# Optimization experiments

Measured on AMD Instinct MI355X. Metric: run time of the kernel, lower is better.

The kernel has to match this reference:

```python
import jax, jax.numpy as jnp
import numpy as np

B, S, D, H = 4, 2048, 1024, 4096  # batch, seq, d_model, mlp hidden
EPS = 1e-12  # F.normalize eps


def _linear(x, W, b):
    return x @ W.T + b


def setup_inputs() -> dict:
    key = jax.random.key(0)
    ks = jax.random.split(key, 14)
    s = lambda d: 1.0 / np.sqrt(d)
    return {
        "x": jax.random.normal(ks[0], (B, S, D), dtype=jnp.float32),
        "Wq": jax.random.normal(ks[1], (D, D), dtype=jnp.float32) * s(D),
        "bq": jax.random.normal(ks[2], (D,), dtype=jnp.float32) * 0.01,
        "Wk": jax.random.normal(ks[3], (D, D), dtype=jnp.float32) * s(D),
        "bk": jax.random.normal(ks[4], (D,), dtype=jnp.float32) * 0.01,
        "Wv": jax.random.normal(ks[5], (D, D), dtype=jnp.float32) * s(D),
        "bv": jax.random.normal(ks[6], (D,), dtype=jnp.float32) * 0.01,
        "W1": jax.random.normal(ks[7], (D, D), dtype=jnp.float32) * s(D),
        "b1": jax.random.normal(ks[8], (D,), dtype=jnp.float32) * 0.01,
        "W2": jax.random.normal(ks[9], (H, D), dtype=jnp.float32) * s(D),
        "b2": jax.random.normal(ks[10], (H,), dtype=jnp.float32) * 0.01,
        "W3": jax.random.normal(ks[11], (D, H), dtype=jnp.float32) * s(H),
        "b3": jax.random.normal(ks[12], (D,), dtype=jnp.float32) * 0.01,
    }


def reference(x, Wq, bq, Wk, bk, Wv, bv, W1, b1, W2, b2, W3, b3):
    Q = _linear(x, Wq, bq)  # [B,S,D]
    K = _linear(x, Wk, bk)
    V = _linear(x, Wv, bv)
    # L2-normalize along feature dim (F.normalize, p=2, dim=2)
    Q = Q / jnp.maximum(jnp.linalg.norm(Q, axis=2, keepdims=True), EPS)
    K = K / jnp.maximum(jnp.linalg.norm(K, axis=2, keepdims=True), EPS)
    sim = jnp.einsum("bqd,bkd->bqk", Q, K)  # cosine similarities [B,S,S]
    attn = jax.nn.softmax(sim, axis=2)
    out = jnp.einsum("bqk,bkd->bqd", attn, V)  # [B,S,D]
    # MLP: Linear->relu->Linear->relu->Linear (dropout identity in eval)
    h = jax.nn.relu(_linear(out, W1, b1))
    h = jax.nn.relu(_linear(h, W2, b2))
    return _linear(h, W3, b3)
```

## Files before the change

### kernel.cpp

```cpp
#include <hip/hip_runtime.h>


using u16 = unsigned short;
using bf16x8 = __attribute__((ext_vector_type(8))) __bf16;
using f32x4  = __attribute__((ext_vector_type(4))) float;

__device__ __forceinline__ u16 f2bf(float f) {
  unsigned u = __float_as_uint(f);
  unsigned r = (u + 0x7FFFu + ((u >> 16) & 1u)) >> 16;
  return (u16)r;
}
__device__ __forceinline__ float bf2f(u16 h) {
  return __uint_as_float(((unsigned)h) << 16);
}

__device__ __forceinline__ void decomp(int lid, int nwg, int gx, int gy,
                                       int gby, int& bx, int& by, int& bz) {
  const int q = nwg >> 3, r = nwg & 7;
  const int xcd = lid & 7, jj = lid >> 3;
  const int wg = (xcd < r ? xcd * (q + 1) : r * (q + 1) + (xcd - r) * q) + jj;
  const int byloc = wg % gby;
  const int t1 = wg / gby;
  bx = t1 % gx;
  const int t2 = t1 / gx;
  const int nb = gy / gby;
  const int band = t2 % nb;
  bz = t2 / nb;
  by = band * gby + byloc;
}

struct CastSegs {
  const float* src[7];
  u16* dst[7];
  long beg[8];
};
__global__ __launch_bounds__(256) void cast_multi_kernel(CastSegs cs) {
  long idx = (long)blockIdx.x * 256 + threadIdx.x;
  if (idx >= cs.beg[7]) return;
  int seg = 0;
#pragma unroll
  for (int s = 1; s < 7; ++s) seg += (idx >= cs.beg[s]) ? 1 : 0;
  const long loc = idx - cs.beg[seg];
  float4 v = reinterpret_cast<const float4*>(cs.src[seg])[loc];
  ushort4 o;
  o.x = f2bf(v.x); o.y = f2bf(v.y); o.z = f2bf(v.z); o.w = f2bf(v.w);
  reinterpret_cast<ushort4*>(cs.dst[seg])[loc] = o;
}

__global__ __launch_bounds__(256) void l2norm2_kernel(
    const u16* __restrict__ Qi, const u16* __restrict__ Ki,
    u16* __restrict__ Qo, u16* __restrict__ Ko) {
  __shared__ float red[4];
  long row = blockIdx.x;
  const u16* in;
  u16* out;
  if (row < 8192) { in = Qi + row * 1024; out = Qo + row * 1024; }
  else            { in = Ki + (row - 8192) * 1024; out = Ko + (row - 8192) * 1024; }
  const int tid = threadIdx.x, lane = tid & 63, wave = tid >> 6;
  ushort4 h = *reinterpret_cast<const ushort4*>(in + tid * 4);
  float x0 = bf2f(h.x), x1 = bf2f(h.y), x2 = bf2f(h.z), x3 = bf2f(h.w);
  float ss = x0 * x0 + x1 * x1 + x2 * x2 + x3 * x3;
#pragma unroll
  for (int o = 32; o; o >>= 1) ss += __shfl_xor(ss, o);
  if (lane == 0) red[wave] = ss;
  __syncthreads();
  ss = red[0] + red[1] + red[2] + red[3];
  float s = 1.0f / fmaxf(sqrtf(ss), 1e-12f);
  ushort4 o;
  o.x = f2bf(x0 * s); o.y = f2bf(x1 * s); o.z = f2bf(x2 * s); o.w = f2bf(x3 * s);
  *reinterpret_cast<ushort4*>(out + tid * 4) = o;
}

__global__ void transpose_kernel(const u16* __restrict__ in, u16* __restrict__ out,
                                 int rows, int cols) {
  __shared__ u16 t[32][33];
  const int c0 = blockIdx.x * 32, r0 = blockIdx.y * 32;
  const long off = (long)blockIdx.z * rows * cols;
  const u16* ib = in + off;
  u16* ob = out + off;
  const int tx = threadIdx.x, ty = threadIdx.y;
#pragma unroll
  for (int j = 0; j < 4; ++j)
    t[ty + j * 8][tx] = ib[(long)(r0 + ty + j * 8) * cols + c0 + tx];
  __syncthreads();
#pragma unroll
  for (int j = 0; j < 4; ++j)
    ob[(long)(c0 + ty + j * 8) * rows + r0 + tx] = t[tx][ty + j * 8];
}

__global__ __launch_bounds__(256) void softmax_kernel(
    const u16* __restrict__ in, u16* __restrict__ out) {
  __shared__ float red[4];
  long row = blockIdx.x;
  const int tid = threadIdx.x, lane = tid & 63, wave = tid >> 6;
  const u16* p = in + row * 2048 + tid * 8;
  ushort4 h0 = *reinterpret_cast<const ushort4*>(p);
  ushort4 h1 = *reinterpret_cast<const ushort4*>(p + 4);
  float v[8];
  v[0] = bf2f(h0.x); v[1] = bf2f(h0.y); v[2] = bf2f(h0.z); v[3] = bf2f(h0.w);
  v[4] = bf2f(h1.x); v[5] = bf2f(h1.y); v[6] = bf2f(h1.z); v[7] = bf2f(h1.w);
  float m = v[0];
#pragma unroll
  for (int i = 1; i < 8; ++i) m = fmaxf(m, v[i]);
#pragma unroll
  for (int o = 32; o; o >>= 1) m = fmaxf(m, __shfl_xor(m, o));
  if (lane == 0) red[wave] = m;
  __syncthreads();
  m = fmaxf(fmaxf(red[0], red[1]), fmaxf(red[2], red[3]));
  float s = 0.0f;
#pragma unroll
  for (int i = 0; i < 8; ++i) { v[i] = __expf(v[i] - m); s += v[i]; }
#pragma unroll
  for (int o = 32; o; o >>= 1) s += __shfl_xor(s, o);
  __syncthreads();
  if (lane == 0) red[wave] = s;
  __syncthreads();
  s = red[0] + red[1] + red[2] + red[3];
  float inv = 1.0f / s;
  ushort4 o0, o1;
  o0.x = f2bf(v[0] * inv); o0.y = f2bf(v[1] * inv);
  o0.z = f2bf(v[2] * inv); o0.w = f2bf(v[3] * inv);
  o1.x = f2bf(v[4] * inv); o1.y = f2bf(v[5] * inv);
  o1.z = f2bf(v[6] * inv); o1.w = f2bf(v[7] * inv);
  *reinterpret_cast<ushort4*>(out + row * 2048 + tid * 8) = o0;
  *reinterpret_cast<ushort4*>(out + row * 2048 + tid * 8 + 4) = o1;
}

struct Frags { bf16x8 a[4][2]; bf16x8 b[4][2]; };

template <int MODE>
__global__ __launch_bounds__(256, 2) void gemmo(
    const u16* __restrict__ A, const u16* __restrict__ Bw,
    const float* __restrict__ bias, void* __restrict__ Cout,
    const float* __restrict__ bias2, void* __restrict__ Cout2,
    const float* __restrict__ bias3, void* __restrict__ Cout3,
    int N, int K, long batchA, long batchB, long batchC, int relu,
    int gx, int gy, int gby) {
  constexpr int ASZ = 128 * 64;
  constexpr int BSZ = 128 * 64;
  __shared__ u16 lds[2 * (ASZ + BSZ)];
  u16* const ldsA = lds;
  u16* const ldsB = lds + 2 * ASZ;

  int bx, by, bz;
  decomp(blockIdx.x, gridDim.x, gx, gy, gby, bx, by, bz);

  const int tid = threadIdx.x, wave = tid >> 6, lane = tid & 63;
  const int wr = wave >> 1, wc = wave & 1;
  const int fr = lane & 15, hi = lane >> 4;

  const long Abase = bz * batchA + (long)by * 128 * K;
  const long Bbase = bz * batchB + (long)bx * 128 * K;

  int aoff[4][2], boff[4][2];
#pragma unroll
  for (int m = 0; m < 4; ++m) {
    const int row = wr * 64 + m * 16 + fr;
#pragma unroll
    for (int ks = 0; ks < 2; ++ks)
      aoff[m][ks] = row * 64 + (((ks * 4 + hi) ^ (row & 7)) * 8);
  }
#pragma unroll
  for (int n = 0; n < 4; ++n) {
    const int row = wc * 64 + n * 16 + fr;
#pragma unroll
    for (int ks = 0; ks < 2; ++ks)
      boff[n][ks] = row * 64 + (((ks * 4 + hi) ^ (row & 7)) * 8);
  }

  const int rA = tid >> 3;
  const int g8 = (((tid & 7) ^ ((tid >> 3) & 7)) * 8);
  long asrc[4], bsrc[4];
#pragma unroll
  for (int rr = 0; rr < 4; ++rr) {
    asrc[rr] = Abase + (long)(rr * 32 + rA) * K + g8;
    bsrc[rr] = Bbase + (long)(rr * 32 + rA) * K + g8;
  }

#define STAGE_A(bufp, rr, k0)                                                  \
  __builtin_amdgcn_global_load_lds(                                            \
      (const __attribute__((address_space(1))) void*)(A + asrc[rr] + (k0)),    \
      (__attribute__((address_space(3))) void*)((bufp) + (rr) * 2048 + tid * 8), \
      16, 0, 0)
#define STAGE_B(bufp, rr, k0)                                                  \
  __builtin_amdgcn_global_load_lds(                                            \
      (const __attribute__((address_space(1))) void*)(Bw + bsrc[rr] + (k0)),   \
      (__attribute__((address_space(3))) void*)((bufp) + (rr) * 2048 + tid * 8), \
      16, 0, 0)
#define STAGE_TILE(T)                                                          \
  {                                                                            \
    u16* sA_ = ldsA + ((T) & 1) * ASZ;                                         \
    u16* sB_ = ldsB + ((T) & 1) * BSZ;                                         \
    const int k0_ = (T) << 6;                                                  \
    STAGE_A(sA_, 0, k0_); STAGE_A(sA_, 1, k0_);                                \
    STAGE_A(sA_, 2, k0_); STAGE_A(sA_, 3, k0_);                                \
    STAGE_B(sB_, 0, k0_); STAGE_B(sB_, 1, k0_);                                \
    STAGE_B(sB_, 2, k0_); STAGE_B(sB_, 3, k0_);                                \
  }
#define READ_FRAGS(F, T)                                                       \
  {                                                                            \
    u16* rA_ = ldsA + ((T) & 1) * ASZ;                                         \
    u16* rB_ = ldsB + ((T) & 1) * BSZ;                                         \
    _Pragma("unroll") for (int m = 0; m < 4; ++m)                              \
    _Pragma("unroll") for (int ks = 0; ks < 2; ++ks)                           \
      F.a[m][ks] = *reinterpret_cast<const bf16x8*>(&rA_[aoff[m][ks]]);        \
    _Pragma("unroll") for (int n = 0; n < 4; ++n)                              \
    _Pragma("unroll") for (int ks = 0; ks < 2; ++ks)                           \
      F.b[n][ks] = *reinterpret_cast<const bf16x8*>(&rB_[boff[n][ks]]);        \
  }
#define RA_ITER(T, FC, FN)                                                     \
  {                                                                            \
    if ((T) + 2 < NT) STAGE_TILE((T) + 2)                                      \
    if ((T) + 1 < NT) {                                                        \
      if ((T) + 2 < NT) asm volatile("s_waitcnt vmcnt(8)" ::: "memory");       \
      else              asm volatile("s_waitcnt vmcnt(0)" ::: "memory");       \
      __builtin_amdgcn_s_barrier();                                            \
      READ_FRAGS(FN, (T) + 1)                                                  \
      __builtin_amdgcn_s_barrier();                                            \
    }                                                                          \
    __builtin_amdgcn_s_setprio(1);                                             \
    _Pragma("unroll") for (int ks = 0; ks < 2; ++ks)                           \
    _Pragma("unroll") for (int m = 0; m < 4; ++m)                              \
    _Pragma("unroll") for (int n = 0; n < 4; ++n)                              \
      acc[m][n] = __builtin_amdgcn_mfma_f32_16x16x32_bf16(                     \
          FC.a[m][ks], FC.b[n][ks], acc[m][n], 0, 0, 0);                       \
    __builtin_amdgcn_s_setprio(0);                                             \
  }

  const int NT = K >> 6;

  f32x4 acc[4][4] = {};
  Frags fA, fB;

  STAGE_TILE(0)
  STAGE_TILE(1)
  asm volatile("s_waitcnt vmcnt(8)" ::: "memory");
  __builtin_amdgcn_s_barrier();
  READ_FRAGS(fA, 0)
  asm volatile("s_waitcnt lgkmcnt(0)" ::: "memory");
  __builtin_amdgcn_sched_barrier(0);
  __builtin_amdgcn_s_barrier();

  for (int t = 0; t < NT; t += 2) {
    RA_ITER(t, fA, fB)
    RA_ITER(t + 1, fB, fA)
  }
#undef STAGE_A
#undef STAGE_B
#undef STAGE_TILE
#undef READ_FRAGS
#undef RA_ITER

  const long cbase = bz * batchC;
  const int crow = by * 128;
  int ccol = bx * 128;
  const float* bp = bias;
  void* cp = Cout;
  constexpr bool obf = (MODE == 1) || (MODE == 2);
  int Nst = N;
  if constexpr (MODE == 2) {
    const int sel = ccol >> 10;
    if (sel == 1) { bp = bias2; cp = Cout2; }
    else if (sel == 2) { bp = bias3; cp = Cout3; }
    ccol &= 1023;
    Nst = 1024;
  }
#pragma unroll
  for (int m = 0; m < 4; ++m) {
    const int r0 = crow + wr * 64 + m * 16 + hi * 4;
#pragma unroll
    for (int n = 0; n < 4; ++n) {
      const int c = ccol + wc * 64 + n * 16 + fr;
      const float bb = bp ? bp[c] : 0.0f;
#pragma unroll
      for (int j = 0; j < 4; ++j) {
        float v = acc[m][n][j] + bb;
        if (relu) v = fmaxf(v, 0.0f);
        const long idx = cbase + (long)(r0 + j) * Nst + c;
        if (obf) ((u16*)cp)[idx] = f2bf(v);
        else     ((float*)cp)[idx] = v;
      }
    }
  }
}

extern "C" void kernel_launch(void* const* d_in, const int* in_sizes, int n_in,
                              void* d_out, int out_size, void* d_ws, size_t ws_size,
                              hipStream_t stream) {
  (void)in_sizes; (void)n_in; (void)out_size; (void)ws_size;
  const float* x  = (const float*)d_in[0];
  const float* Wq = (const float*)d_in[1];
  const float* bq = (const float*)d_in[2];
  const float* Wk = (const float*)d_in[3];
  const float* bk = (const float*)d_in[4];
  const float* Wv = (const float*)d_in[5];
  const float* bv = (const float*)d_in[6];
  const float* W1 = (const float*)d_in[7];
  const float* b1 = (const float*)d_in[8];
  const float* W2 = (const float*)d_in[9];
  const float* b2 = (const float*)d_in[10];
  const float* W3 = (const float*)d_in[11];
  const float* b3 = (const float*)d_in[12];

  char* ws = (char*)d_ws;
  const size_t MB = 1u << 20;
  u16* Qbf  = (u16*)(ws + 0);
  u16* Kbf  = Qbf + 8388608;
  u16* h2   = (u16*)(ws + 0);
  u16* xbf = (u16*)(ws + 64 * MB);
  u16* Vbf = xbf + (size_t)8192 * 1024;
  u16* P   = (u16*)(ws + 64 * MB);
  u16* Wq_b = (u16*)(ws + 96 * MB);
  u16* Wk_b = Wq_b + 1048576;
  u16* Wv_b = Wk_b + 1048576;
  u16* W1_b = Wv_b + 1048576;
  u16* W2_b = W1_b + 1048576;
  u16* W3_b = W2_b + 4194304;
  u16* Qn = (u16*)(ws + 120 * MB);
  u16* Kn = Qn + 8388608;
  u16* Vt = Kn + 8388608;
  u16* attnout = Qn;
  u16* h1      = Kn;

  CastSegs cs;
  cs.src[0] = x;  cs.dst[0] = xbf;
  cs.src[1] = Wq; cs.dst[1] = Wq_b;
  cs.src[2] = Wk; cs.dst[2] = Wk_b;
  cs.src[3] = Wv; cs.dst[3] = Wv_b;
  cs.src[4] = W1; cs.dst[4] = W1_b;
  cs.src[5] = W2; cs.dst[5] = W2_b;
  cs.src[6] = W3; cs.dst[6] = W3_b;
  long szs[7] = {2097152, 262144, 262144, 262144, 262144, 1048576, 1048576};
  long acc0 = 0;
  for (int i = 0; i < 7; ++i) { cs.beg[i] = acc0; acc0 += szs[i]; }
  cs.beg[7] = acc0;
  cast_multi_kernel<<<dim3((unsigned)((acc0 + 255) / 256)), 256, 0, stream>>>(cs);

  dim3 blk(256);
  gemmo<2><<<dim3(24 * 64), blk, 0, stream>>>(
      xbf, Wq_b, bq, Qbf, bk, Kbf, bv, Vbf, 3072, 1024, 0, 0, 0, 0, 24, 64, 8);
  l2norm2_kernel<<<16384, 256, 0, stream>>>(Qbf, Kbf, Qn, Kn);
  transpose_kernel<<<dim3(32, 64, 4), dim3(32, 8), 0, stream>>>(Vbf, Vt, 2048, 1024);
  gemmo<1><<<dim3(16 * 16 * 4), blk, 0, stream>>>(
      Qn, Kn, nullptr, P, nullptr, nullptr, nullptr, nullptr,
      2048, 1024, 2097152L, 2097152L, 4194304L, 0, 16, 16, 8);
  softmax_kernel<<<8192, 256, 0, stream>>>(P, P);
  gemmo<1><<<dim3(8 * 16 * 4), blk, 0, stream>>>(
      P, Vt, nullptr, attnout, nullptr, nullptr, nullptr, nullptr,
      1024, 2048, 4194304L, 2097152L, 2097152L, 0, 8, 16, 8);
  gemmo<1><<<dim3(8 * 64), blk, 0, stream>>>(
      attnout, W1_b, b1, h1, nullptr, nullptr, nullptr, nullptr,
      1024, 1024, 0, 0, 0, 1, 8, 64, 16);
  gemmo<1><<<dim3(32 * 64), blk, 0, stream>>>(
      h1, W2_b, b2, h2, nullptr, nullptr, nullptr, nullptr,
      4096, 1024, 0, 0, 0, 1, 32, 64, 8);
  gemmo<0><<<dim3(8 * 64), blk, 0, stream>>>(
      h2, W3_b, b3, (float*)d_out, nullptr, nullptr, nullptr, nullptr,
      1024, 4096, 0, 0, 0, 0, 8, 64, 16);
}
```

Baseline: 365.7 us.

## Rework GEMM to triple-buffered K=32 pipeline and fold L2 norms into QK epilogue

The GEMM mainloop now uses BK=32 with a three-buffer LDS ring, a smaller LDS footprint, and launch bounds raised to four blocks per CU, replacing the BK=64 double-buffered register-prefetch scheme. The L2 normalization no longer writes normalized Q/K copies. It computes per-row inverse norms, and a new QK GEMM mode scales each output by row and column inverse norms in its epilogue. This is meant to remove a full read/write pass over Q and K and to raise occupancy, at the cost of more barriers per K and a slightly different rounding order (normalizing after the bf16 matmul).

```diff
diff --git a/kernel.cpp b/kernel.cpp
--- a/kernel.cpp
+++ b/kernel.cpp
@@ -47,15 +47,15 @@
   reinterpret_cast<ushort4*>(cs.dst[seg])[loc] = o;
 }
 
-__global__ __launch_bounds__(256) void l2norm2_kernel(
+__global__ __launch_bounds__(256) void norms_kernel(
     const u16* __restrict__ Qi, const u16* __restrict__ Ki,
-    u16* __restrict__ Qo, u16* __restrict__ Ko) {
+    float* __restrict__ rq, float* __restrict__ rk) {
   __shared__ float red[4];
   long row = blockIdx.x;
   const u16* in;
-  u16* out;
-  if (row < 8192) { in = Qi + row * 1024; out = Qo + row * 1024; }
-  else            { in = Ki + (row - 8192) * 1024; out = Ko + (row - 8192) * 1024; }
+  float* out;
+  if (row < 8192) { in = Qi + row * 1024; out = rq + row; }
+  else            { in = Ki + (row - 8192) * 1024; out = rk + (row - 8192); }
   const int tid = threadIdx.x, lane = tid & 63, wave = tid >> 6;
   ushort4 h = *reinterpret_cast<const ushort4*>(in + tid * 4);
   float x0 = bf2f(h.x), x1 = bf2f(h.y), x2 = bf2f(h.z), x3 = bf2f(h.w);
@@ -64,11 +64,10 @@
   for (int o = 32; o; o >>= 1) ss += __shfl_xor(ss, o);
   if (lane == 0) red[wave] = ss;
   __syncthreads();
-  ss = red[0] + red[1] + red[2] + red[3];
-  float s = 1.0f / fmaxf(sqrtf(ss), 1e-12f);
-  ushort4 o;
-  o.x = f2bf(x0 * s); o.y = f2bf(x1 * s); o.z = f2bf(x2 * s); o.w = f2bf(x3 * s);
-  *reinterpret_cast<ushort4*>(out + tid * 4) = o;
+  if (tid == 0) {
+    ss = red[0] + red[1] + red[2] + red[3];
+    *out = 1.0f / fmaxf(sqrtf(ss), 1e-12f);
+  }
 }
 
 __global__ void transpose_kernel(const u16* __restrict__ in, u16* __restrict__ out,
@@ -126,21 +125,16 @@
   *reinterpret_cast<ushort4*>(out + row * 2048 + tid * 8 + 4) = o1;
 }
 
-struct Frags { bf16x8 a[4][2]; bf16x8 b[4][2]; };
-
 template <int MODE>
-__global__ __launch_bounds__(256, 2) void gemmo(
+__global__ __launch_bounds__(256, 4) void gemmo2(
     const u16* __restrict__ A, const u16* __restrict__ Bw,
     const float* __restrict__ bias, void* __restrict__ Cout,
     const float* __restrict__ bias2, void* __restrict__ Cout2,
     const float* __restrict__ bias3, void* __restrict__ Cout3,
     int N, int K, long batchA, long batchB, long batchC, int relu,
     int gx, int gy, int gby) {
-  constexpr int ASZ = 128 * 64;
-  constexpr int BSZ = 128 * 64;
-  __shared__ u16 lds[2 * (ASZ + BSZ)];
-  u16* const ldsA = lds;
-  u16* const ldsB = lds + 2 * ASZ;
+  constexpr int BUF = 128 * 32;
+  __shared__ u16 lds[3 * 2 * BUF];
 
   int bx, by, bz;
   decomp(blockIdx.x, gridDim.x, gx, gy, gby, bx, by, bz);
@@ -152,111 +146,91 @@
   const long Abase = bz * batchA + (long)by * 128 * K;
   const long Bbase = bz * batchB + (long)bx * 128 * K;
 
-  int aoff[4][2], boff[4][2];
+  int aoff[4], boff[4];
 #pragma unroll
   for (int m = 0; m < 4; ++m) {
     const int row = wr * 64 + m * 16 + fr;
-#pragma unroll
-    for (int ks = 0; ks < 2; ++ks)
-      aoff[m][ks] = row * 64 + (((ks * 4 + hi) ^ (row & 7)) * 8);
+    aoff[m] = row * 32 + ((hi ^ ((row >> 1) & 3)) * 8);
   }
 #pragma unroll
   for (int n = 0; n < 4; ++n) {
     const int row = wc * 64 + n * 16 + fr;
-#pragma unroll
-    for (int ks = 0; ks < 2; ++ks)
-      boff[n][ks] = row * 64 + (((ks * 4 + hi) ^ (row & 7)) * 8);
-  }
-
-  const int rA = tid >> 3;
-  const int g8 = (((tid & 7) ^ ((tid >> 3) & 7)) * 8);
-  long asrc[4], bsrc[4];
-#pragma unroll
-  for (int rr = 0; rr < 4; ++rr) {
-    asrc[rr] = Abase + (long)(rr * 32 + rA) * K + g8;
-    bsrc[rr] = Bbase + (long)(rr * 32 + rA) * K + g8;
-  }
-
-#define STAGE_A(bufp, rr, k0)                                                  \
-  __builtin_amdgcn_global_load_lds(                                            \
-      (const __attribute__((address_space(1))) void*)(A + asrc[rr] + (k0)),    \
-      (__attribute__((address_space(3))) void*)((bufp) + (rr) * 2048 + tid * 8), \
-      16, 0, 0)
-#define STAGE_B(bufp, rr, k0)                                                  \
-  __builtin_amdgcn_global_load_lds(                                            \
-      (const __attribute__((address_space(1))) void*)(Bw + bsrc[rr] + (k0)),   \
-      (__attribute__((address_space(3))) void*)((bufp) + (rr) * 2048 + tid * 8), \
-      16, 0, 0)
-#define STAGE_TILE(T)                                                          \
+    boff[n] = row * 32 + ((hi ^ ((row >> 1) & 3)) * 8);
+  }
+
+  const int srow = tid >> 2;
+  const int g8 = (((tid & 3) ^ ((tid >> 3) & 3)) * 8);
+  long asrc[2], bsrc[2];
+#pragma unroll
+  for (int rr = 0; rr < 2; ++rr) {
+    asrc[rr] = Abase + (long)(rr * 64 + srow) * K + g8;
+    bsrc[rr] = Bbase + (long)(rr * 64 + srow) * K + g8;
+  }
+
+#define STAGE_TILE(bufp, T)                                                    \
   {                                                                            \
-    u16* sA_ = ldsA + ((T) & 1) * ASZ;                                         \
-    u16* sB_ = ldsB + ((T) & 1) * BSZ;                                         \
-    const int k0_ = (T) << 6;                                                  \
-    STAGE_A(sA_, 0, k0_); STAGE_A(sA_, 1, k0_);                                \
-    STAGE_A(sA_, 2, k0_); STAGE_A(sA_, 3, k0_);                                \
-    STAGE_B(sB_, 0, k0_); STAGE_B(sB_, 1, k0_);                                \
-    STAGE_B(sB_, 2, k0_); STAGE_B(sB_, 3, k0_);                                \
-  }
-#define READ_FRAGS(F, T)                                                       \
-  {                                                                            \
-    u16* rA_ = ldsA + ((T) & 1) * ASZ;                                         \
-    u16* rB_ = ldsB + ((T) & 1) * BSZ;                                         \
-    _Pragma("unroll") for (int m = 0; m < 4; ++m)                              \
-    _Pragma("unroll") for (int ks = 0; ks < 2; ++ks)                           \
-      F.a[m][ks] = *reinterpret_cast<const bf16x8*>(&rA_[aoff[m][ks]]);        \
-    _Pragma("unroll") for (int n = 0; n < 4; ++n)                              \
-    _Pragma("unroll") for (int ks = 0; ks < 2; ++ks)                           \
-      F.b[n][ks] = *reinterpret_cast<const bf16x8*>(&rB_[boff[n][ks]]);        \
-  }
-#define RA_ITER(T, FC, FN)                                                     \
-  {                                                                            \
-    if ((T) + 2 < NT) STAGE_TILE((T) + 2)                                      \
-    if ((T) + 1 < NT) {                                                        \
-      if ((T) + 2 < NT) asm volatile("s_waitcnt vmcnt(8)" ::: "memory");       \
-      else              asm volatile("s_waitcnt vmcnt(0)" ::: "memory");       \
-      __builtin_amdgcn_s_barrier();                                            \
-      READ_FRAGS(FN, (T) + 1)                                                  \
-      __builtin_amdgcn_s_barrier();                                            \
-    }                                                                          \
-    __builtin_amdgcn_s_setprio(1);                                             \
-    _Pragma("unroll") for (int ks = 0; ks < 2; ++ks)                           \
-    _Pragma("unroll") for (int m = 0; m < 4; ++m)                              \
-    _Pragma("unroll") for (int n = 0; n < 4; ++n)                              \
-      acc[m][n] = __builtin_amdgcn_mfma_f32_16x16x32_bf16(                     \
-          FC.a[m][ks], FC.b[n][ks], acc[m][n], 0, 0, 0);                       \
-    __builtin_amdgcn_s_setprio(0);                                             \
-  }
-
-  const int NT = K >> 6;
+    const int k0_ = (T) << 5;                                                  \
+    __builtin_amdgcn_global_load_lds(                                          \
+        (const __attribute__((address_space(1))) void*)(A + asrc[0] + k0_),    \
+        (__attribute__((address_space(3))) void*)((bufp) + tid * 8), 16, 0, 0);\
+    __builtin_amdgcn_global_load_lds(                                          \
+        (const __attribute__((address_space(1))) void*)(A + asrc[1] + k0_),    \
+        (__attribute__((address_space(3))) void*)((bufp) + 2048 + tid * 8),    \
+        16, 0, 0);                                                             \
+    __builtin_amdgcn_global_load_lds(                                          \
+        (const __attribute__((address_space(1))) void*)(Bw + bsrc[0] + k0_),   \
+        (__attribute__((address_space(3))) void*)((bufp) + BUF + tid * 8),     \
+        16, 0, 0);                                                             \
+    __builtin_amdgcn_global_load_lds(                                          \
+        (const __attribute__((address_space(1))) void*)(Bw + bsrc[1] + k0_),   \
+        (__attribute__((address_space(3))) void*)((bufp) + BUF + 2048 + tid * 8), \
+        16, 0, 0);                                                             \
+  }
+
+  const int NT = K >> 5;
+
+  u16* pR = lds;
+  u16* pN = lds + 2 * BUF;
+  u16* pS = lds + 4 * BUF;
+
+  STAGE_TILE(pR, 0)
+  STAGE_TILE(pN, 1)
+  asm volatile("s_waitcnt vmcnt(4)" ::: "memory");
+  __builtin_amdgcn_s_barrier();
 
   f32x4 acc[4][4] = {};
-  Frags fA, fB;
-
-  STAGE_TILE(0)
-  STAGE_TILE(1)
-  asm volatile("s_waitcnt vmcnt(8)" ::: "memory");
-  __builtin_amdgcn_s_barrier();
-  READ_FRAGS(fA, 0)
-  asm volatile("s_waitcnt lgkmcnt(0)" ::: "memory");
-  __builtin_amdgcn_sched_barrier(0);
-  __builtin_amdgcn_s_barrier();
-
-  for (int t = 0; t < NT; t += 2) {
-    RA_ITER(t, fA, fB)
-    RA_ITER(t + 1, fB, fA)
-  }
-#undef STAGE_A
-#undef STAGE_B
+
+  for (int t = 0; t < NT; ++t) {
+    const bool st = (t + 2) < NT;
+    if (st) STAGE_TILE(pS, t + 2)
+    bf16x8 a[4], b[4];
+#pragma unroll
+    for (int m = 0; m < 4; ++m)
+      a[m] = *reinterpret_cast<const bf16x8*>(&pR[aoff[m]]);
+#pragma unroll
+    for (int n = 0; n < 4; ++n)
+      b[n] = *reinterpret_cast<const bf16x8*>(&pR[BUF + boff[n]]);
+    __builtin_amdgcn_s_setprio(1);
+#pragma unroll
+    for (int m = 0; m < 4; ++m)
+#pragma unroll
+      for (int n = 0; n < 4; ++n)
+        acc[m][n] = __builtin_amdgcn_mfma_f32_16x16x32_bf16(
+            a[m], b[n], acc[m][n], 0, 0, 0);
+    __builtin_amdgcn_s_setprio(0);
+    if (st) asm volatile("s_waitcnt vmcnt(4)" ::: "memory");
+    else if (t + 1 < NT) asm volatile("s_waitcnt vmcnt(0)" ::: "memory");
+    __builtin_amdgcn_s_barrier();
+    u16* tmp = pR; pR = pN; pN = pS; pS = tmp;
+  }
 #undef STAGE_TILE
-#undef READ_FRAGS
-#undef RA_ITER
 
   const long cbase = bz * batchC;
   const int crow = by * 128;
   int ccol = bx * 128;
   const float* bp = bias;
   void* cp = Cout;
-  constexpr bool obf = (MODE == 1) || (MODE == 2);
+  constexpr bool obf = (MODE != 0);
   int Nst = N;
   if constexpr (MODE == 2) {
     const int sel = ccol >> 10;
@@ -271,11 +245,18 @@
 #pragma unroll
     for (int n = 0; n < 4; ++n) {
       const int c = ccol + wc * 64 + n * 16 + fr;
-      const float bb = bp ? bp[c] : 0.0f;
+      float bb = 0.0f, cscale = 1.0f;
+      if constexpr (MODE == 3) { cscale = bias2[bz * 2048 + c]; }
+      else { bb = bp ? bp[c] : 0.0f; }
 #pragma unroll
       for (int j = 0; j < 4; ++j) {
-        float v = acc[m][n][j] + bb;
-        if (relu) v = fmaxf(v, 0.0f);
+        float v;
+        if constexpr (MODE == 3)
+          v = acc[m][n][j] * bias[bz * 2048 + r0 + j] * cscale;
+        else {
+          v = acc[m][n][j] + bb;
+          if (relu) v = fmaxf(v, 0.0f);
+        }
         const long idx = cbase + (long)(r0 + j) * Nst + c;
         if (obf) ((u16*)cp)[idx] = f2bf(v);
         else     ((float*)cp)[idx] = v;
@@ -304,9 +285,11 @@
 
   char* ws = (char*)d_ws;
   const size_t MB = 1u << 20;
-  u16* Qbf  = (u16*)(ws + 0);
-  u16* Kbf  = Qbf + 8388608;
-  u16* h2   = (u16*)(ws + 0);
+  u16* Qbf = (u16*)(ws + 0);
+  u16* Kbf = Qbf + 8388608;
+  float* rq = (float*)(ws + 32 * MB);
+  float* rk = rq + 8192;
+  u16* h2  = (u16*)(ws + 0);
   u16* xbf = (u16*)(ws + 64 * MB);
   u16* Vbf = xbf + (size_t)8192 * 1024;
   u16* P   = (u16*)(ws + 64 * MB);
@@ -316,11 +299,9 @@
   u16* W1_b = Wv_b + 1048576;
   u16* W2_b = W1_b + 1048576;
   u16* W3_b = W2_b + 4194304;
-  u16* Qn = (u16*)(ws + 120 * MB);
-  u16* Kn = Qn + 8388608;
-  u16* Vt = Kn + 8388608;
-  u16* attnout = Qn;
-  u16* h1      = Kn;
+  u16* attnout = (u16*)(ws + 120 * MB);
+  u16* h1      = attnout + 8388608;
+  u16* Vt      = h1 + 8388608;
 
   CastSegs cs;
   cs.src[0] = x;  cs.dst[0] = xbf;
@@ -337,24 +318,24 @@
   cast_multi_kernel<<<dim3((unsigned)((acc0 + 255) / 256)), 256, 0, stream>>>(cs);
 
   dim3 blk(256);
-  gemmo<2><<<dim3(24 * 64), blk, 0, stream>>>(
+  gemmo2<2><<<dim3(24 * 64), blk, 0, stream>>>(
       xbf, Wq_b, bq, Qbf, bk, Kbf, bv, Vbf, 3072, 1024, 0, 0, 0, 0, 24, 64, 8);
-  l2norm2_kernel<<<16384, 256, 0, stream>>>(Qbf, Kbf, Qn, Kn);
+  norms_kernel<<<16384, 256, 0, stream>>>(Qbf, Kbf, rq, rk);
   transpose_kernel<<<dim3(32, 64, 4), dim3(32, 8), 0, stream>>>(Vbf, Vt, 2048, 1024);
-  gemmo<1><<<dim3(16 * 16 * 4), blk, 0, stream>>>(
-      Qn, Kn, nullptr, P, nullptr, nullptr, nullptr, nullptr,
+  gemmo2<3><<<dim3(16 * 16 * 4), blk, 0, stream>>>(
+      Qbf, Kbf, rq, P, rk, nullptr, nullptr, nullptr,
       2048, 1024, 2097152L, 2097152L, 4194304L, 0, 16, 16, 8);
   softmax_kernel<<<8192, 256, 0, stream>>>(P, P);
-  gemmo<1><<<dim3(8 * 16 * 4), blk, 0, stream>>>(
+  gemmo2<1><<<dim3(8 * 16 * 4), blk, 0, stream>>>(
       P, Vt, nullptr, attnout, nullptr, nullptr, nullptr, nullptr,
       1024, 2048, 4194304L, 2097152L, 2097152L, 0, 8, 16, 8);
-  gemmo<1><<<dim3(8 * 64), blk, 0, stream>>>(
+  gemmo2<1><<<dim3(8 * 64), blk, 0, stream>>>(
       attnout, W1_b, b1, h1, nullptr, nullptr, nullptr, nullptr,
       1024, 1024, 0, 0, 0, 1, 8, 64, 16);
-  gemmo<1><<<dim3(32 * 64), blk, 0, stream>>>(
+  gemmo2<1><<<dim3(32 * 64), blk, 0, stream>>>(
       h1, W2_b, b2, h2, nullptr, nullptr, nullptr, nullptr,
       4096, 1024, 0, 0, 0, 1, 32, 64, 8);
-  gemmo<0><<<dim3(8 * 64), blk, 0, stream>>>(
+  gemmo2<0><<<dim3(8 * 64), blk, 0, stream>>>(
       h2, W3_b, b3, (float*)d_out, nullptr, nullptr, nullptr, nullptr,
       1024, 4096, 0, 0, 0, 0, 8, 64, 16);
 }
```

After: 390.0 us. 1.07x slower.
